# Kernel optimization log

Measured on AMD Instinct MI355X. Metric: run time of the kernel, lower is better.

The kernel has to match this reference:

```python
import jax, jax.numpy as jnp
import numpy as np
import math

B, S, E, H, L = 16, 512, 256, 4, 2
D = E // H            # head size = 64
MAX_POS = 10
NUM_ITEMS = 50000


def setup_inputs() -> dict:
    key = jax.random.key(0)
    ks = jax.random.split(key, 16)
    s = 0.02
    item_inputs = jax.random.randint(ks[0], (B, S), 0, 2 * NUM_ITEMS + 1)
    item_ids = jax.random.randint(ks[1], (B, S), 0, NUM_ITEMS)
    input_embed = jax.random.normal(ks[2], (2 * NUM_ITEMS + 1, E), jnp.float32) * s
    input_embed = input_embed.at[0].set(0.0)  # padding_idx=0
    query_embed = jax.random.normal(ks[3], (NUM_ITEMS, E), jnp.float32) * s
    pos_key = jax.random.normal(ks[4], (MAX_POS, D), jnp.float32) * s
    pos_value = jax.random.normal(ks[5], (MAX_POS, D), jnp.float32) * s
    Wq = jax.random.normal(ks[6], (L, E, E), jnp.float32) * s
    bq = jnp.zeros((L, E), jnp.float32)
    Wk = jax.random.normal(ks[7], (L, E, E), jnp.float32) * s
    bk = jnp.zeros((L, E), jnp.float32)
    Wv = jax.random.normal(ks[8], (L, E, E), jnp.float32) * s
    bv = jnp.zeros((L, E), jnp.float32)
    Wo = jax.random.normal(ks[9], (L, E, E), jnp.float32) * s
    bo = jnp.zeros((L, E), jnp.float32)
    out_w = jax.random.normal(ks[10], (E, 1), jnp.float32) * s
    out_b = jnp.zeros((1,), jnp.float32)
    return dict(item_inputs=item_inputs, item_ids=item_ids,
                input_embed=input_embed, query_embed=query_embed,
                pos_key=pos_key, pos_value=pos_value,
                Wq=Wq, bq=bq, Wk=Wk, bk=bk, Wv=Wv, bv=bv, Wo=Wo, bo=bo,
                out_w=out_w, out_b=out_b)


def _heads(x, W, b):
    # [B,S,E] @ [E,E] -> [B,H,S,D]
    return (x @ W + b).reshape(B, S, H, D).transpose(0, 2, 1, 3)


def reference(item_inputs, item_ids, input_embed, query_embed, pos_key,
              pos_value, Wq, bq, Wk, bk, Wv, bv, Wo, bo, out_w, out_b):
    x = input_embed[item_inputs]          # [B,S,E]
    q_base = query_embed[item_ids]        # [B,S,E]

    i = jnp.arange(S)
    rel = jnp.clip(i[:, None] - i[None, :], 0, MAX_POS - 1)  # [S,S]
    pk = pos_key[rel]                     # [S,S,D]
    pv = pos_value[rel]                   # [S,S,D]
    causal = i[None, :] > i[:, None]      # future mask [S,S], True = masked
    scale = 1.0 / math.sqrt(D)

    out = x
    for l in range(L):
        qh = _heads(q_base, Wq[l], bq[l])
        kh = _heads(out, Wk[l], bk[l])
        vh = _heads(out, Wv[l], bv[l])
        # relative attention: scores = q.k^T + q.pos_key(i-j)
        scores = jnp.einsum('bhid,bhjd->bhij', qh, kh)
        scores = scores + jnp.einsum('bhid,ijd->bhij', qh, pk)
        scores = scores * scale
        scores = jnp.where(causal[None, None], -1e9, scores)
        p = jax.nn.softmax(scores, axis=-1)  # [B,H,S,S]
        # out_i = sum_j p_ij * (v_j + pos_value(i-j))
        attn = jnp.einsum('bhij,bhjd->bhid', p, vh) \
             + jnp.einsum('bhij,ijd->bhid', p, pv)
        merged = attn.transpose(0, 2, 1, 3).reshape(B, S, E)
        residual = merged @ Wo[l] + bo[l]
        out = out + jax.nn.relu(residual)
    return out @ out_w + out_b            # [B,S,1]
```

## Files before the change

kernel.cpp:

```cpp
#include <hip/hip_runtime.h>
#include <hip/hip_bf16.h>

#define B_ 16
#define S_ 512
#define E_ 256
#define H_ 4
#define D_ 64
#define L_ 2
#define MAXPOS 10
#define HS_ ((size_t)B_ * S_ * E_)

typedef __attribute__((ext_vector_type(8))) short bf16x8;
typedef __attribute__((ext_vector_type(4))) float f32x4;

static __device__ __forceinline__ short f2bf(float f) {
    __hip_bfloat16 h = __float2bfloat16(f);
    return __builtin_bit_cast(short, h);
}

static __device__ __forceinline__ void gload16(const void* g, void* l) {
    __builtin_amdgcn_global_load_lds(
        (const __attribute__((address_space(1))) void*)(g),
        (__attribute__((address_space(3))) void*)(l),
        16, 0, 0);
}

static __device__ __forceinline__ void stage_tile(const char* gbase, char* lds,
                                                  int w, int lane) {
    #pragma unroll
    for (int c = 0; c < 8; ++c) {
        const int L = (w * 8 + c) * 1024 + lane * 16;
        const int src = L ^ (((L >> 9) & 7) << 4);
        gload16(gbase + src, lds + (w * 8 + c) * 1024);
    }
}

static __device__ __forceinline__ void gemm4(const short* As, const short* Bs,
                                             int w, int l15, int l4,
                                             f32x4& a0, f32x4& a1,
                                             f32x4& a2, f32x4& a3) {
    const int sw = (l15 & 7) << 4;
    const int arow = w * 16 + l15;
    const f32x4 z4 = (f32x4){0.f, 0.f, 0.f, 0.f};
    a0 = z4; a1 = z4; a2 = z4; a3 = z4;
    #pragma unroll
    for (int ks = 0; ks < 8; ++ks) {
        const int coff = (ks * 64 + l4 * 16) ^ sw;
        const bf16x8 af = *reinterpret_cast<const bf16x8*>((const char*)As + arow * 512 + coff);
        const bf16x8 b0 = *reinterpret_cast<const bf16x8*>((const char*)Bs + (0 * 16 + l15) * 512 + coff);
        a0 = __builtin_amdgcn_mfma_f32_16x16x32_bf16(af, b0, a0, 0, 0, 0);
        const bf16x8 b1 = *reinterpret_cast<const bf16x8*>((const char*)Bs + (1 * 16 + l15) * 512 + coff);
        a1 = __builtin_amdgcn_mfma_f32_16x16x32_bf16(af, b1, a1, 0, 0, 0);
        const bf16x8 b2 = *reinterpret_cast<const bf16x8*>((const char*)Bs + (2 * 16 + l15) * 512 + coff);
        a2 = __builtin_amdgcn_mfma_f32_16x16x32_bf16(af, b2, a2, 0, 0, 0);
        const bf16x8 b3 = *reinterpret_cast<const bf16x8*>((const char*)Bs + (3 * 16 + l15) * 512 + coff);
        a3 = __builtin_amdgcn_mfma_f32_16x16x32_bf16(af, b3, a3, 0, 0, 0);
    }
}

static __device__ __forceinline__ void gemm_compute(const short* As, const short* Bs,
                                                    f32x4* acc, int w, int l15, int l4) {
    gemm4(As, Bs, w, l15, l4, acc[0], acc[1], acc[2], acc[3]);
}

__global__ __launch_bounds__(256) void setup_kernel(
    const int* __restrict__ item_inputs, const int* __restrict__ item_ids,
    const float* __restrict__ input_embed, const float* __restrict__ query_embed,
    const float* __restrict__ Wq, const float* __restrict__ Wk,
    const float* __restrict__ Wv, const float* __restrict__ Wo,
    const float* __restrict__ out_b,
    short* __restrict__ outb, short* __restrict__ qbb,
    short* __restrict__ Wt, float* __restrict__ y)
{
    const int tid = threadIdx.x;
    const int bx = blockIdx.x;
    if (bx < 512) {
        const int rr = tid >> 4, c0 = (tid & 15) * 16;
        const int row = bx * 16 + rr;
        const int ii = item_inputs[row];
        const int qi = item_ids[row];
        const float* xs = input_embed + (size_t)ii * E_ + c0;
        const float* qs = query_embed + (size_t)qi * E_ + c0;
        short* ob = outb + (size_t)row * E_ + c0;
        short* qb = qbb + (size_t)row * E_ + c0;
        #pragma unroll
        for (int q = 0; q < 4; ++q) {
            const float4 xv = reinterpret_cast<const float4*>(xs)[q];
            const float4 qv = reinterpret_cast<const float4*>(qs)[q];
            short4 xb = { f2bf(xv.x), f2bf(xv.y), f2bf(xv.z), f2bf(xv.w) };
            short4 qb4 = { f2bf(qv.x), f2bf(qv.y), f2bf(qv.z), f2bf(qv.w) };
            reinterpret_cast<short4*>(ob)[q] = xb;
            reinterpret_cast<short4*>(qb)[q] = qb4;
        }
        return;
    }
    const int pb = bx - 512;
    if (pb < 128) {
        __shared__ short tt[64 * 72];
        const int mId = pb >> 4;
        const int l = mId >> 2, which = mId & 3;
        const float* src = (which == 0 ? Wq : which == 1 ? Wk : which == 2 ? Wv : Wo)
                         + (size_t)l * E_ * E_;
        const int tr = (pb >> 2) & 3;
        const int tc = pb & 3;
        {
            const int kl = tid >> 2;
            const int nq = (tid & 3) * 16;
            const float* sp = src + (size_t)(tr * 64 + kl) * E_ + tc * 64 + nq;
            #pragma unroll
            for (int q = 0; q < 4; ++q) {
                const float4 v = reinterpret_cast<const float4*>(sp)[q];
                tt[(nq + q * 4 + 0) * 72 + kl] = f2bf(v.x);
                tt[(nq + q * 4 + 1) * 72 + kl] = f2bf(v.y);
                tt[(nq + q * 4 + 2) * 72 + kl] = f2bf(v.z);
                tt[(nq + q * 4 + 3) * 72 + kl] = f2bf(v.w);
            }
        }
        __syncthreads();
        {
            const int nl = tid >> 2;
            const int kq = (tid & 3) * 16;
            short* dst = Wt + (size_t)mId * 65536 + (size_t)(tc * 64 + nl) * E_ + tr * 64 + kq;
            *reinterpret_cast<bf16x8*>(&dst[0]) = *reinterpret_cast<const bf16x8*>(&tt[nl * 72 + kq]);
            *reinterpret_cast<bf16x8*>(&dst[8]) = *reinterpret_cast<const bf16x8*>(&tt[nl * 72 + kq + 8]);
        }
    } else if (pb == 128) {
        const float yb = out_b[0];
        for (int i = tid; i < 8192; i += 256) y[i] = yb;
    }
}

__global__ __launch_bounds__(256) void qkv0_kernel(
    const short* __restrict__ qbb, const short* __restrict__ outb,
    const short* __restrict__ Wt, const float* __restrict__ bq,
    const float* __restrict__ bk, const float* __restrict__ bv,
    const float* __restrict__ bq1, short* __restrict__ Qb,
    short* __restrict__ Qb1)
{
    __shared__ __align__(16) short As[64 * 256];
    __shared__ __align__(16) short Bs[64 * 256];
    const int bm = blockIdx.x, bn = blockIdx.y, z = blockIdx.z;
    const int tid = threadIdx.x;
    const int lane = tid & 63, w = tid >> 6;
    const int l15 = lane & 15, l4 = lane >> 4;

    const short* A = (z == 1 || z == 2) ? outb : qbb;
    const short* W = (z == 3) ? (Wt + (size_t)4 * 65536) : (Wt + (size_t)z * 65536);
    const float* bias = (z == 0) ? bq : (z == 1) ? bk : (z == 2) ? bv : bq1;

    stage_tile((const char*)A + (size_t)bm * 32768, (char*)As, w, lane);
    stage_tile((const char*)W + (size_t)bn * 32768, (char*)Bs, w, lane);
    __syncthreads();

    f32x4 acc[4];
    gemm_compute(As, Bs, acc, w, l15, l4);

    short* Cz = (z == 3) ? Qb1 : Qb + (size_t)z * HS_;
    #pragma unroll
    for (int nf = 0; nf < 4; ++nf) {
        const int col = bn * 64 + nf * 16 + l15;
        const float bb = bias[col];
        #pragma unroll
        for (int reg = 0; reg < 4; ++reg) {
            const int rowg = bm * 64 + w * 16 + l4 * 4 + reg;
            Cz[(size_t)rowg * E_ + col] = f2bf(acc[nf][reg] + bb);
        }
    }
}

__global__ __launch_bounds__(256) void kv1_kernel(
    const short* __restrict__ outb, const short* __restrict__ Wt1,
    const float* __restrict__ bk1, const float* __restrict__ bv1,
    short* __restrict__ Qb)
{
    __shared__ __align__(16) short As[64 * 256];
    __shared__ __align__(16) short Bs[64 * 256];
    const int bm = blockIdx.x, bn = blockIdx.y, z = blockIdx.z;
    const int tid = threadIdx.x;
    const int lane = tid & 63, w = tid >> 6;
    const int l15 = lane & 15, l4 = lane >> 4;

    const short* W = Wt1 + (size_t)(z + 1) * 65536;
    const float* bias = (z == 0) ? bk1 : bv1;

    stage_tile((const char*)outb + (size_t)bm * 32768, (char*)As, w, lane);
    stage_tile((const char*)W + (size_t)bn * 32768, (char*)Bs, w, lane);
    __syncthreads();

    f32x4 acc[4];
    gemm_compute(As, Bs, acc, w, l15, l4);

    short* Cz = Qb + (size_t)(z + 1) * HS_;
    #pragma unroll
    for (int nf = 0; nf < 4; ++nf) {
        const int col = bn * 64 + nf * 16 + l15;
        const float bb = bias[col];
        #pragma unroll
        for (int reg = 0; reg < 4; ++reg) {
            const int rowg = bm * 64 + w * 16 + l4 * 4 + reg;
            Cz[(size_t)rowg * E_ + col] = f2bf(acc[nf][reg] + bb);
        }
    }
}

__global__ __launch_bounds__(256) void o0_kernel(
    const short* __restrict__ mgb, const short* __restrict__ Wo_t,
    const float* __restrict__ bo0, const int* __restrict__ item_inputs,
    const float* __restrict__ input_embed, float* __restrict__ outf,
    short* __restrict__ outb)
{
    __shared__ __align__(16) short As[64 * 256];
    __shared__ __align__(16) short Bs[64 * 256];
    const int bm = blockIdx.x, bn = blockIdx.y;
    const int tid = threadIdx.x;
    const int lane = tid & 63, w = tid >> 6;
    const int l15 = lane & 15, l4 = lane >> 4;

    stage_tile((const char*)mgb + (size_t)bm * 32768, (char*)As, w, lane);
    stage_tile((const char*)Wo_t + (size_t)bn * 32768, (char*)Bs, w, lane);
    __syncthreads();

    f32x4 acc[4];
    gemm_compute(As, Bs, acc, w, l15, l4);

    #pragma unroll
    for (int reg = 0; reg < 4; ++reg) {
        const int rowg = bm * 64 + w * 16 + l4 * 4 + reg;
        const int ii = item_inputs[rowg];
        const float* emb = input_embed + (size_t)ii * E_;
        #pragma unroll
        for (int nf = 0; nf < 4; ++nf) {
            const int col = bn * 64 + nf * 16 + l15;
            const size_t idx = (size_t)rowg * E_ + col;
            const float o = emb[col] + fmaxf(acc[nf][reg] + bo0[col], 0.0f);
            outf[idx] = o;
            outb[idx] = f2bf(o);
        }
    }
}

__global__ __launch_bounds__(256) void attn_kernel(
    const short* __restrict__ Q, const short* __restrict__ K,
    const short* __restrict__ V, const float* __restrict__ pos_key,
    const float* __restrict__ pos_value, short* __restrict__ merged)
{
    __shared__ __align__(16) short Qs[64 * 72];
    __shared__ __align__(16) short Ks[2][64 * 64];
    __shared__ __align__(16) short Vts[2][4656];
    __shared__ __align__(16) short Pl[4 * 16 * 72];
    __shared__ __align__(16) short Pk[16 * 72];
    __shared__ float pv_sh[MAXPOS * 64];
    __shared__ float qpk_sh[64 * 16];
    __shared__ float pdiag[64 * 9];

    const int bid = blockIdx.x;
    const int half = bid >> 8;
    const int g = bid & 255;
    const int tp = g & 3;
    const int bh = g >> 2;
    const int it = half ? tp : 7 - tp;
    const int h = bh & 3;
    const int b = bh >> 2;
    const int tid = threadIdx.x;
    const int lane = tid & 63;
    const int w = tid >> 6;
    const int l15 = lane & 15;
    const int l4  = lane >> 4;
    const int rloc  = l4 * 4;
    const int rbase = w * 16 + rloc;
    const int swl = (l15 & 7) << 4;
    const float SC = 0.18033688f;

    const size_t boff = (size_t)(b * S_) * E_ + h * D_;

    for (int idx = tid; idx < MAXPOS * 64; idx += 256) pv_sh[idx] = pos_value[idx];
    for (int idx = tid; idx < 64 * 9; idx += 256) pdiag[idx] = 0.0f;
    for (int idx = tid; idx < 16 * 64; idx += 256) {
        const int r = idx >> 6, d = idx & 63;
        Pk[r * 72 + d] = (r < MAXPOS) ? f2bf(pos_key[r * 64 + d]) : (short)0;
    }
    {
        const int row = tid >> 2, dq = (tid & 3) * 16;
        const short* qp = &Q[boff + (size_t)(it * 64 + row) * E_ + dq];
        *reinterpret_cast<bf16x8*>(&Qs[row * 72 + dq]) = *reinterpret_cast<const bf16x8*>(qp);
        *reinterpret_cast<bf16x8*>(&Qs[row * 72 + dq + 8]) = *reinterpret_cast<const bf16x8*>(qp + 8);
    }

    auto stageKV = [&](int jt, int buf) {
        const char* Kb = (const char*)(K + boff + (size_t)(jt * 64) * E_);
        #pragma unroll
        for (int c = 0; c < 2; ++c) {
            const int chunk = w * 2 + c;
            const int row = chunk * 8 + (lane >> 3);
            const int col = (lane & 7) * 16;
            const int src = row * 512 + (col ^ ((row & 7) << 4));
            gload16(Kb + src, (char*)Ks[buf] + chunk * 1024);
        }
        const int row = tid >> 2, dq = (tid & 3) * 16;
        const short* vp = &V[boff + (size_t)(jt * 64 + row) * E_ + dq];
        const bf16x8 v0 = *reinterpret_cast<const bf16x8*>(vp);
        const bf16x8 v1 = *reinterpret_cast<const bf16x8*>(vp + 8);
        const int skew = (tid & 3) * 32 + row * 2;
        #pragma unroll
        for (int e = 0; e < 8; ++e) {
            *(short*)((char*)Vts[buf] + (dq + e) * 144 + skew) = v0[e];
            *(short*)((char*)Vts[buf] + (dq + 8 + e) * 144 + skew) = v1[e];
        }
    };

    stageKV(0, 0);
    __syncthreads();

    bf16x8 aq[2];
    #pragma unroll
    for (int ks = 0; ks < 2; ++ks)
        aq[ks] = *reinterpret_cast<const bf16x8*>(&Qs[(w * 16 + l15) * 72 + ks * 32 + 8 * l4]);

    f32x4 cq = (f32x4){0.f, 0.f, 0.f, 0.f};
    #pragma unroll
    for (int ks = 0; ks < 2; ++ks) {
        const bf16x8 bpk = *reinterpret_cast<const bf16x8*>(&Pk[l15 * 72 + ks * 32 + 8 * l4]);
        cq = __builtin_amdgcn_mfma_f32_16x16x32_bf16(aq[ks], bpk, cq, 0, 0, 0);
    }
    float q9[4];
    #pragma unroll
    for (int r = 0; r < 4; ++r) {
        qpk_sh[(rbase + r) * 16 + l15] = cq[r] * SC;
        q9[r] = __shfl(cq[r], l4 * 16 + 9, 64) * SC;
    }

    f32x4 accv[4];
    #pragma unroll
    for (int nf = 0; nf < 4; ++nf) accv[nf] = (f32x4){0.f, 0.f, 0.f, 0.f};
    float ls[4] = {0.f, 0.f, 0.f, 0.f};

    for (int jt = 0; jt <= it; ++jt) {
        const int cur = jt & 1;
        if (jt < it) stageKV(jt + 1, cur ^ 1);

        const bool near = (jt >= it - 1);
        #pragma unroll
        for (int nf = 0; nf < 4; ++nf) {
            f32x4 c = (f32x4){0.f, 0.f, 0.f, 0.f};
            const int jrow = nf * 16 + l15;
            const bf16x8 bk0 = *reinterpret_cast<const bf16x8*>(
                (const char*)Ks[cur] + jrow * 128 + ((l4 * 16) ^ swl));
            const bf16x8 bk1 = *reinterpret_cast<const bf16x8*>(
                (const char*)Ks[cur] + jrow * 128 + ((64 + l4 * 16) ^ swl));
            c = __builtin_amdgcn_mfma_f32_16x16x32_bf16(aq[0], bk0, c, 0, 0, 0);
            c = __builtin_amdgcn_mfma_f32_16x16x32_bf16(aq[1], bk1, c, 0, 0, 0);
            const int j = jt * 64 + nf * 16 + l15;
            #pragma unroll
            for (int r = 0; r < 4; ++r) {
                float pp;
                if (near) {
                    const int i = it * 64 + rbase + r;
                    const int rel = i - j;
                    if (rel < 0) pp = 0.0f;
                    else {
                        const int rc = rel < 9 ? rel : 9;
                        pp = exp2f(fmaf(c[r], SC, qpk_sh[(rbase + r) * 16 + rc]));
                        if (rel < 9) pdiag[(rbase + r) * 9 + rel] = pp;
                    }
                } else {
                    pp = exp2f(fmaf(c[r], SC, q9[r]));
                }
                ls[r] += pp;
                Pl[w * 1152 + (rloc + r) * 72 + nf * 16 + l15] = f2bf(pp);
            }
        }
        #pragma unroll
        for (int ks = 0; ks < 2; ++ks) {
            const bf16x8 pa = *reinterpret_cast<const bf16x8*>(
                &Pl[w * 1152 + l15 * 72 + ks * 32 + 8 * l4]);
            #pragma unroll
            for (int nf = 0; nf < 4; ++nf) {
                const int d = nf * 16 + l15;
                const bf16x8 bv = *reinterpret_cast<const bf16x8*>(
                    (const char*)Vts[cur] + d * 144 + nf * 32 + ks * 64 + l4 * 16);
                accv[nf] = __builtin_amdgcn_mfma_f32_16x16x32_bf16(pa, bv, accv[nf], 0, 0, 0);
            }
        }
        __syncthreads();
    }

    #pragma unroll
    for (int m = 1; m < 16; m <<= 1) {
        #pragma unroll
        for (int r = 0; r < 4; ++r) ls[r] += __shfl_xor(ls[r], m, 64);
    }

    #pragma unroll
    for (int r = 0; r < 4; ++r) {
        const int rowl = rbase + r;
        const float inv = 1.0f / ls[r];
        #pragma unroll
        for (int nf = 0; nf < 4; ++nf) {
            const int col = nf * 16 + l15;
            const float pv9 = pv_sh[9 * 64 + col];
            float extra = ls[r] * pv9;
            #pragma unroll
            for (int rr = 0; rr < 9; ++rr)
                extra += pdiag[rowl * 9 + rr] * (pv_sh[rr * 64 + col] - pv9);
            merged[boff + (size_t)(it * 64 + rowl) * E_ + col] =
                f2bf((accv[nf][r] + extra) * inv);
        }
    }
}

__global__ __launch_bounds__(256) void o1final_kernel(
    const short* __restrict__ mgb, const short* __restrict__ Wt7,
    const float* __restrict__ bo1, const float* __restrict__ outf,
    const float* __restrict__ fw, float* __restrict__ y)
{
    __shared__ __align__(16) short As[64 * 256];
    __shared__ __align__(16) short Bs[64 * 256];
    const int bm = blockIdx.x, bn = blockIdx.y;
    const int tid = threadIdx.x;
    const int lane = tid & 63, w = tid >> 6;
    const int l15 = lane & 15, l4 = lane >> 4;

    stage_tile((const char*)mgb + (size_t)bm * 32768, (char*)As, w, lane);
    stage_tile((const char*)Wt7 + (size_t)bn * 32768, (char*)Bs, w, lane);
    __syncthreads();

    f32x4 acc[4];
    gemm_compute(As, Bs, acc, w, l15, l4);

    float s[4] = {0.f, 0.f, 0.f, 0.f};
    #pragma unroll
    for (int nf = 0; nf < 4; ++nf) {
        const int col = bn * 64 + nf * 16 + l15;
        const float bb = bo1[col];
        const float fwv = fw[col];
        #pragma unroll
        for (int reg = 0; reg < 4; ++reg) {
            const int rowg = bm * 64 + w * 16 + l4 * 4 + reg;
            const float o = outf[(size_t)rowg * E_ + col] + fmaxf(acc[nf][reg] + bb, 0.0f);
            s[reg] += o * fwv;
        }
    }
    #pragma unroll
    for (int m = 1; m < 16; m <<= 1) {
        #pragma unroll
        for (int reg = 0; reg < 4; ++reg) s[reg] += __shfl_xor(s[reg], m, 64);
    }
    if (l15 == 0) {
        #pragma unroll
        for (int reg = 0; reg < 4; ++reg)
            atomicAdd(&y[bm * 64 + w * 16 + l4 * 4 + reg], s[reg]);
    }
}

extern "C" void kernel_launch(void* const* d_in, const int* in_sizes, int n_in,
                              void* d_out, int out_size, void* d_ws, size_t ws_size,
                              hipStream_t stream) {
    const int*   item_inputs = (const int*)d_in[0];
    const int*   item_ids    = (const int*)d_in[1];
    const float* input_embed = (const float*)d_in[2];
    const float* query_embed = (const float*)d_in[3];
    const float* pos_key     = (const float*)d_in[4];
    const float* pos_value   = (const float*)d_in[5];
    const float* Wq = (const float*)d_in[6];
    const float* bq = (const float*)d_in[7];
    const float* Wk = (const float*)d_in[8];
    const float* bk = (const float*)d_in[9];
    const float* Wv = (const float*)d_in[10];
    const float* bv = (const float*)d_in[11];
    const float* Wo = (const float*)d_in[12];
    const float* bo = (const float*)d_in[13];
    const float* out_w = (const float*)d_in[14];
    const float* out_b = (const float*)d_in[15];
    float* y = (float*)d_out;

    char* w8 = (char*)d_ws;
    float* outf = (float*)(w8);
    short* outb = (short*)(w8 + ((size_t)8  << 20));
    short* qbb  = (short*)(w8 + ((size_t)12 << 20));
    short* Qb   = (short*)(w8 + ((size_t)16 << 20));
    short* mgb  = (short*)(w8 + ((size_t)28 << 20));
    short* Wt   = (short*)(w8 + ((size_t)32 << 20));
    short* Qb1  = (short*)(w8 + ((size_t)34 << 20));

    setup_kernel<<<641, 256, 0, stream>>>(
        item_inputs, item_ids, input_embed, query_embed,
        Wq, Wk, Wv, Wo, out_b, outb, qbb, Wt, y);

    qkv0_kernel<<<dim3(128, 4, 4), 256, 0, stream>>>(
        qbb, outb, Wt, bq, bk, bv, bq + E_, Qb, Qb1);
    attn_kernel<<<512, 256, 0, stream>>>(
        Qb, Qb + HS_, Qb + 2 * HS_, pos_key, pos_value, mgb);
    o0_kernel<<<dim3(128, 4), 256, 0, stream>>>(
        mgb, Wt + (size_t)3 * 65536, bo, item_inputs, input_embed, outf, outb);

    kv1_kernel<<<dim3(128, 4, 2), 256, 0, stream>>>(
        outb, Wt + (size_t)4 * 65536, bk + E_, bv + E_, Qb);
    attn_kernel<<<512, 256, 0, stream>>>(
        Qb1, Qb + HS_, Qb + 2 * HS_, pos_key, pos_value, mgb);
    o1final_kernel<<<dim3(128, 4), 256, 0, stream>>>(
        mgb, Wt + (size_t)7 * 65536, bo + E_, outf, out_w, y);
}
```

Before: 90.57 us.

## Defer V tile LDS writes past compute and raise MFMA wave priority

Splits the K/V staging so the next V tile's global loads go into registers at the top of each iteration and are written to the transposed LDS buffer only after the current tile's P·V MFMAs. This hides global-load latency behind compute instead of stalling on it before the QK MFMAs. The QK MFMAs are batched ahead of the softmax loop, and s_setprio is raised around MFMA sections. The trailing barrier is skipped on the last iteration. The cost is extra VGPRs to hold the in-flight V data, which could lower occupancy.

```diff
diff --git a/kernel.cpp b/kernel.cpp
--- a/kernel.cpp
+++ b/kernel.cpp
@@ -273,20 +273,9 @@
 
     const size_t boff = (size_t)(b * S_) * E_ + h * D_;
 
-    for (int idx = tid; idx < MAXPOS * 64; idx += 256) pv_sh[idx] = pos_value[idx];
-    for (int idx = tid; idx < 64 * 9; idx += 256) pdiag[idx] = 0.0f;
-    for (int idx = tid; idx < 16 * 64; idx += 256) {
-        const int r = idx >> 6, d = idx & 63;
-        Pk[r * 72 + d] = (r < MAXPOS) ? f2bf(pos_key[r * 64 + d]) : (short)0;
-    }
-    {
-        const int row = tid >> 2, dq = (tid & 3) * 16;
-        const short* qp = &Q[boff + (size_t)(it * 64 + row) * E_ + dq];
-        *reinterpret_cast<bf16x8*>(&Qs[row * 72 + dq]) = *reinterpret_cast<const bf16x8*>(qp);
-        *reinterpret_cast<bf16x8*>(&Qs[row * 72 + dq + 8]) = *reinterpret_cast<const bf16x8*>(qp + 8);
-    }
-
-    auto stageKV = [&](int jt, int buf) {
+    const int vrow = tid >> 2, vdq = (tid & 3) * 16;
+    const int vskew = (tid & 3) * 32 + vrow * 2;
+    auto issueK = [&](int jt, int buf) {
         const char* Kb = (const char*)(K + boff + (size_t)(jt * 64) * E_);
         #pragma unroll
         for (int c = 0; c < 2; ++c) {
@@ -296,19 +285,37 @@
             const int src = row * 512 + (col ^ ((row & 7) << 4));
             gload16(Kb + src, (char*)Ks[buf] + chunk * 1024);
         }
+    };
+    auto issueV = [&](int jt, bf16x8& v0, bf16x8& v1) {
+        const short* vp = &V[boff + (size_t)(jt * 64 + vrow) * E_ + vdq];
+        v0 = *reinterpret_cast<const bf16x8*>(vp);
+        v1 = *reinterpret_cast<const bf16x8*>(vp + 8);
+    };
+    auto writeV = [&](int buf, const bf16x8& v0, const bf16x8& v1) {
+        #pragma unroll
+        for (int e = 0; e < 8; ++e) {
+            *(short*)((char*)Vts[buf] + (vdq + e) * 144 + vskew) = v0[e];
+            *(short*)((char*)Vts[buf] + (vdq + 8 + e) * 144 + vskew) = v1[e];
+        }
+    };
+
+    issueK(0, 0);
+    bf16x8 vc0, vc1;
+    issueV(0, vc0, vc1);
+
+    for (int idx = tid; idx < MAXPOS * 64; idx += 256) pv_sh[idx] = pos_value[idx];
+    for (int idx = tid; idx < 64 * 9; idx += 256) pdiag[idx] = 0.0f;
+    for (int idx = tid; idx < 16 * 64; idx += 256) {
+        const int r = idx >> 6, d = idx & 63;
+        Pk[r * 72 + d] = (r < MAXPOS) ? f2bf(pos_key[r * 64 + d]) : (short)0;
+    }
+    {
         const int row = tid >> 2, dq = (tid & 3) * 16;
-        const short* vp = &V[boff + (size_t)(jt * 64 + row) * E_ + dq];
-        const bf16x8 v0 = *reinterpret_cast<const bf16x8*>(vp);
-        const bf16x8 v1 = *reinterpret_cast<const bf16x8*>(vp + 8);
-        const int skew = (tid & 3) * 32 + row * 2;
-        #pragma unroll
-        for (int e = 0; e < 8; ++e) {
-            *(short*)((char*)Vts[buf] + (dq + e) * 144 + skew) = v0[e];
-            *(short*)((char*)Vts[buf] + (dq + 8 + e) * 144 + skew) = v1[e];
-        }
-    };
-
-    stageKV(0, 0);
+        const short* qp = &Q[boff + (size_t)(it * 64 + row) * E_ + dq];
+        *reinterpret_cast<bf16x8*>(&Qs[row * 72 + dq]) = *reinterpret_cast<const bf16x8*>(qp);
+        *reinterpret_cast<bf16x8*>(&Qs[row * 72 + dq + 8]) = *reinterpret_cast<const bf16x8*>(qp + 8);
+    }
+    writeV(0, vc0, vc1);
     __syncthreads();
 
     bf16x8 aq[2];
@@ -336,19 +343,30 @@
 
     for (int jt = 0; jt <= it; ++jt) {
         const int cur = jt & 1;
-        if (jt < it) stageKV(jt + 1, cur ^ 1);
-
-        const bool near = (jt >= it - 1);
+        bf16x8 vn0, vn1;
+        if (jt < it) {
+            issueK(jt + 1, cur ^ 1);
+            issueV(jt + 1, vn0, vn1);
+        }
+
+        f32x4 cs[4];
+        __builtin_amdgcn_s_setprio(1);
         #pragma unroll
         for (int nf = 0; nf < 4; ++nf) {
-            f32x4 c = (f32x4){0.f, 0.f, 0.f, 0.f};
             const int jrow = nf * 16 + l15;
             const bf16x8 bk0 = *reinterpret_cast<const bf16x8*>(
                 (const char*)Ks[cur] + jrow * 128 + ((l4 * 16) ^ swl));
             const bf16x8 bk1 = *reinterpret_cast<const bf16x8*>(
                 (const char*)Ks[cur] + jrow * 128 + ((64 + l4 * 16) ^ swl));
+            f32x4 c = (f32x4){0.f, 0.f, 0.f, 0.f};
             c = __builtin_amdgcn_mfma_f32_16x16x32_bf16(aq[0], bk0, c, 0, 0, 0);
-            c = __builtin_amdgcn_mfma_f32_16x16x32_bf16(aq[1], bk1, c, 0, 0, 0);
+            cs[nf] = __builtin_amdgcn_mfma_f32_16x16x32_bf16(aq[1], bk1, c, 0, 0, 0);
+        }
+        __builtin_amdgcn_s_setprio(0);
+
+        const bool near = (jt >= it - 1);
+        #pragma unroll
+        for (int nf = 0; nf < 4; ++nf) {
             const int j = jt * 64 + nf * 16 + l15;
             #pragma unroll
             for (int r = 0; r < 4; ++r) {
@@ -359,16 +377,18 @@
                     if (rel < 0) pp = 0.0f;
                     else {
                         const int rc = rel < 9 ? rel : 9;
-                        pp = exp2f(fmaf(c[r], SC, qpk_sh[(rbase + r) * 16 + rc]));
+                        pp = exp2f(fmaf(cs[nf][r], SC, qpk_sh[(rbase + r) * 16 + rc]));
                         if (rel < 9) pdiag[(rbase + r) * 9 + rel] = pp;
                     }
                 } else {
-                    pp = exp2f(fmaf(c[r], SC, q9[r]));
+                    pp = exp2f(fmaf(cs[nf][r], SC, q9[r]));
                 }
                 ls[r] += pp;
                 Pl[w * 1152 + (rloc + r) * 72 + nf * 16 + l15] = f2bf(pp);
             }
         }
+
+        __builtin_amdgcn_s_setprio(1);
         #pragma unroll
         for (int ks = 0; ks < 2; ++ks) {
             const bf16x8 pa = *reinterpret_cast<const bf16x8*>(
@@ -381,7 +401,12 @@
                 accv[nf] = __builtin_amdgcn_mfma_f32_16x16x32_bf16(pa, bv, accv[nf], 0, 0, 0);
             }
         }
-        __syncthreads();
+        __builtin_amdgcn_s_setprio(0);
+
+        if (jt < it) {
+            writeV(cur ^ 1, vn0, vn1);
+            __syncthreads();
+        }
     }
 
     #pragma unroll
```

Measured after the change: 91.48 us. Within noise of the previous version (+1.0%).
